# Kernel optimization log

Hardware: AMD Instinct MI355X
Metric: run time of the kernel (lower is better)

## Reference

```python
import jax, jax.numpy as jnp
import numpy as np

BASIS_PRIMES = (2, 3, 5, 7, 11, 13, 17, 19, 23, 29)


def _build_resonance(max_seq):
    # p-adic valuations v_p(n) for n = 1..max_seq, each basis prime (vectorized LUT build)
    n = np.arange(1, max_seq + 1, dtype=np.int64)
    vals = np.zeros((max_seq, len(BASIS_PRIMES)), dtype=np.float32)
    for j, p in enumerate(BASIS_PRIMES):
        m = n.copy()
        while True:
            div = (m % p) == 0
            if not div.any():
                break
            vals[div, j] += 1.0
            m = np.where(div, m // p, m)
    # resonance(a,b) = sum_i min(v_{p_i}(a), v_{p_i}(b))  -> [T, T]
    res = np.zeros((max_seq, max_seq), dtype=np.float32)
    for j in range(len(BASIS_PRIMES)):
        vj = vals[:, j]
        res += np.minimum(vj[:, None], vj[None, :])
    causal = np.tril(np.ones((max_seq, max_seq), dtype=bool))
    allowed = ((res > 0) | np.eye(max_seq, dtype=bool)) & causal
    bias = (np.log1p(res) * allowed).astype(np.float32)
    return bias, allowed


def setup_inputs() -> dict:
    B, T, d_model, head_size, max_seq = 8, 2048, 1024, 128, 2048
    key = jax.random.key(0)
    kx, kq, kk, kv = jax.random.split(key, 4)
    bound = 1.0 / np.sqrt(d_model)  # torch Linear default init range
    x = jax.random.normal(kx, (B, T, d_model), dtype=jnp.float32)
    Wq = jax.random.uniform(kq, (head_size, d_model), jnp.float32, -bound, bound)
    Wk = jax.random.uniform(kk, (head_size, d_model), jnp.float32, -bound, bound)
    Wv = jax.random.uniform(kv, (head_size, d_model), jnp.float32, -bound, bound)
    bias, allowed = _build_resonance(max_seq)
    return {
        "x": x, "Wq": Wq, "Wk": Wk, "Wv": Wv,
        "resonance_bias": jnp.asarray(bias),
        "allowed": jnp.asarray(allowed),
    }


def reference(x, Wq, Wk, Wv, resonance_bias, allowed):
    B, T, C = x.shape
    q = jnp.einsum('btc,hc->bth', x, Wq)
    k = jnp.einsum('btc,hc->bth', x, Wk)
    v = jnp.einsum('btc,hc->bth', x, Wv)
    # NOTE: original scales by C**-0.5 where C = d_model (input channels)
    wei = jnp.einsum('bth,bsh->bts', q, k) * (C ** -0.5)
    wei = wei + resonance_bias[:T, :T]
    neg = jnp.finfo(wei.dtype).min
    wei = jnp.where(allowed[:T, :T], wei, neg)
    wei = jax.nn.softmax(wei, axis=-1)  # dropout is identity in eval mode
    return jnp.einsum('bts,bsh->bth', wei, v)
```

## Files before the change

kernel.cpp:

```cpp
#include <hip/hip_runtime.h>
#include <hip/hip_bf16.h>
#include <stdint.h>

typedef float f32x4  __attribute__((ext_vector_type(4)));
typedef short s16x8  __attribute__((ext_vector_type(8)));
typedef short s16x4  __attribute__((ext_vector_type(4)));
typedef unsigned short u16x8 __attribute__((ext_vector_type(8)));

#define MFMA16(A,B,C) __builtin_amdgcn_mfma_f32_16x16x32_bf16((A),(B),(C),0,0,0)

__device__ __forceinline__ short f2bf(float f) {
    uint32_t u = __float_as_uint(f);
    u += 0x7FFFu + ((u >> 16) & 1u);
    return (short)(u >> 16);
}
__device__ __forceinline__ float bf2f(unsigned short u) {
    return __uint_as_float(((uint32_t)u) << 16);
}
__device__ __forceinline__ int cum_jobs(int qt) {
  int h = qt >> 1;
  return (qt & 1) ? (h + 1) * (h + 1) : h * (h + 1);
}

#define OFF_PB   0u
#define OFF_WPK  8388608u
#define OFF_PQ   9175040u
#define OFF_PK   13369344u
#define OFF_PV   17563648u
#define OFF_PML  21757952u
#define OFF_PO   22863872u
#define WS_SPLIT 60096512u

__global__ __launch_bounds__(256) void pack_misc_kernel(
    const float* __restrict__ wq, const float* __restrict__ wk,
    const float* __restrict__ wv, const float* __restrict__ bias,
    short* __restrict__ Wpk, short* __restrict__ pb) {
  const int tid = threadIdx.x, wid = tid >> 6, lane = tid & 63;
  const int g = lane >> 4, c4 = lane & 15;
  if (blockIdx.x < 192) {
    const int idx = blockIdx.x * 4 + wid;
    const int im = idx >> 8, rest = idx & 255;
    const int ntl = rest >> 5, k32 = rest & 31;
    const float* w = (im == 0) ? wq : (im == 1) ? wk : wv;
    const float* p = w + (size_t)(ntl * 16 + c4) * 1024 + k32 * 32 + 4 * g;
    f32x4 lo = *(const f32x4*)p;
    f32x4 hi = *(const f32x4*)(p + 16);
    s16x8 o = { f2bf(lo[0]), f2bf(lo[1]), f2bf(lo[2]), f2bf(lo[3]),
                f2bf(hi[0]), f2bf(hi[1]), f2bf(hi[2]), f2bf(hi[3]) };
    *(s16x8*)(Wpk + (size_t)idx * 512 + lane * 8) = o;
  } else {
    const int idx = (blockIdx.x - 192) * 4 + wid;
    const int t16 = idx >> 6, s32 = idx & 63;
    const int t = t16 * 16 + c4;
    const int sb = s32 * 32 + 4 * g;
    const float* p = bias + (size_t)t * 2048 + sb;
    f32x4 lo = *(const f32x4*)p;
    f32x4 hi = *(const f32x4*)(p + 16);
    s16x8 o;
    #pragma unroll
    for (int i = 0; i < 4; ++i) {
      int s0 = sb + i, s1 = sb + 16 + i;
      bool ok0 = (s0 <= t) && (s0 == t || lo[i] > 0.f);
      bool ok1 = (s1 <= t) && (s1 == t || hi[i] > 0.f);
      o[i]     = f2bf(ok0 ? lo[i] : -1e30f);
      o[4 + i] = f2bf(ok1 ? hi[i] : -1e30f);
    }
    *(s16x8*)(pb + (size_t)idx * 512 + lane * 8) = o;
  }
}

__global__ __launch_bounds__(256, 2) void qkv_gemm8_kernel(
    const float* __restrict__ x, const short* __restrict__ Wpk,
    short* __restrict__ pq, short* __restrict__ pk, short* __restrict__ pv) {
  __shared__ short lx[2][1024];
  const int tid = threadIdx.x, wid = tid >> 6, lane = tid & 63;
  const int g = lane >> 4, c4 = lane & 15;
  const int L8 = lane * 8;
  const int t2 = blockIdx.x;
  const int b = t2 >> 6;
  const int srow = tid >> 3, scg = tid & 7;
  const float* xs = x + (size_t)(t2 * 32 + srow) * 1024 + scg * 4;
  const int swoff = (srow >> 4) * 512 + (((scg & 3) * 16 + (srow & 15)) * 8)
                  + (scg >> 2) * 4;
  {
    f32x4 xv = *(const f32x4*)xs;
    s16x4 sv = { f2bf(xv[0]), f2bf(xv[1]), f2bf(xv[2]), f2bf(xv[3]) };
    *(s16x4*)&lx[0][swoff] = sv;
  }
  __syncthreads();

  if (wid < 2) {
    const short* wp = Wpk + (size_t)(wid * 256) * 512 + L8;
    f32x4 acc0[8], acc1[8];
    #pragma unroll
    for (int i = 0; i < 8; ++i) {
      acc0[i] = (f32x4){0.f, 0.f, 0.f, 0.f};
      acc1[i] = (f32x4){0.f, 0.f, 0.f, 0.f};
    }
    for (int k = 0; k < 32; ++k) {
      f32x4 xn;
      if (k < 31) xn = *(const f32x4*)(xs + (size_t)(k + 1) * 32);
      s16x8 wf[8];
      #pragma unroll
      for (int nt = 0; nt < 8; ++nt)
        wf[nt] = *(const s16x8*)(wp + (size_t)(nt * 32 + k) * 512);
      const short* lb = &lx[k & 1][0];
      s16x8 xf0 = *(const s16x8*)(lb + L8);
      s16x8 xf1 = *(const s16x8*)(lb + 512 + L8);
      #pragma unroll
      for (int nt = 0; nt < 8; ++nt) {
        acc0[nt] = MFMA16(wf[nt], xf0, acc0[nt]);
        acc1[nt] = MFMA16(wf[nt], xf1, acc1[nt]);
      }
      if (k < 31) {
        s16x4 sv = { f2bf(xn[0]), f2bf(xn[1]), f2bf(xn[2]), f2bf(xn[3]) };
        *(s16x4*)&lx[(k + 1) & 1][swoff] = sv;
      }
      __syncthreads();
    }
    short* __restrict__ o = wid ? pk : pq;
    const int loc0 = (t2 & 63) * 2;
    #pragma unroll
    for (int f = 0; f < 4; ++f) {
      s16x8 fr0 = { f2bf(acc0[2*f][0]),   f2bf(acc0[2*f][1]),
                    f2bf(acc0[2*f][2]),   f2bf(acc0[2*f][3]),
                    f2bf(acc0[2*f+1][0]), f2bf(acc0[2*f+1][1]),
                    f2bf(acc0[2*f+1][2]), f2bf(acc0[2*f+1][3]) };
      *(s16x8*)(o + (size_t)(b * 512 + loc0 * 4 + f) * 512 + L8) = fr0;
      s16x8 fr1 = { f2bf(acc1[2*f][0]),   f2bf(acc1[2*f][1]),
                    f2bf(acc1[2*f][2]),   f2bf(acc1[2*f][3]),
                    f2bf(acc1[2*f+1][0]), f2bf(acc1[2*f+1][1]),
                    f2bf(acc1[2*f+1][2]), f2bf(acc1[2*f+1][3]) };
      *(s16x8*)(o + (size_t)(b * 512 + (loc0 + 1) * 4 + f) * 512 + L8) = fr1;
    }
  } else {
    const int ntoff = (wid - 2) * 4;
    const short* wp = Wpk + (size_t)(512 + ntoff * 32) * 512 + L8;
    f32x4 acc0[4], acc1[4];
    #pragma unroll
    for (int i = 0; i < 4; ++i) {
      acc0[i] = (f32x4){0.f, 0.f, 0.f, 0.f};
      acc1[i] = (f32x4){0.f, 0.f, 0.f, 0.f};
    }
    for (int k = 0; k < 32; ++k) {
      f32x4 xn;
      if (k < 31) xn = *(const f32x4*)(xs + (size_t)(k + 1) * 32);
      s16x8 wf[4];
      #pragma unroll
      for (int j = 0; j < 4; ++j)
        wf[j] = *(const s16x8*)(wp + (size_t)(j * 32 + k) * 512);
      const short* lb = &lx[k & 1][0];
      s16x8 xf0 = *(const s16x8*)(lb + L8);
      s16x8 xf1 = *(const s16x8*)(lb + 512 + L8);
      #pragma unroll
      for (int j = 0; j < 4; ++j) {
        acc0[j] = MFMA16(xf0, wf[j], acc0[j]);
        acc1[j] = MFMA16(xf1, wf[j], acc1[j]);
      }
      if (k < 31) {
        s16x4 sv = { f2bf(xn[0]), f2bf(xn[1]), f2bf(xn[2]), f2bf(xn[3]) };
        *(s16x4*)&lx[(k + 1) & 1][swoff] = sv;
      }
      __syncthreads();
    }
    const int s32l = t2 & 63;
    #pragma unroll
    for (int j = 0; j < 4; ++j) {
      s16x8 fr = { f2bf(acc0[j][0]), f2bf(acc0[j][1]),
                   f2bf(acc0[j][2]), f2bf(acc0[j][3]),
                   f2bf(acc1[j][0]), f2bf(acc1[j][1]),
                   f2bf(acc1[j][2]), f2bf(acc1[j][3]) };
      *(s16x8*)(pv + (size_t)(b * 512 + s32l * 8 + ntoff + j) * 512 + L8) = fr;
    }
  }
}

template<bool SPLIT>
__global__ __launch_bounds__(128) void attn_kernel(
    const short* __restrict__ pq, const short* __restrict__ pk,
    const short* __restrict__ pv, const short* __restrict__ pb,
    float* __restrict__ out, float* __restrict__ part_ml,
    short* __restrict__ part_o) {
  int qt, c;
  if (SPLIT) {
    const int i = blockIdx.x;
    int h = (int)sqrtf((float)i);
    while (h * h > i) --h;
    while ((h + 1) * (h + 1) <= i) ++h;
    if (i < h * (h + 1)) { qt = 2 * h - 1; c = i - h * h; }
    else                 { qt = 2 * h;     c = i - h * (h + 1); }
  } else {
    qt = blockIdx.x; c = 0;
  }
  const int n = (qt >> 1) + 1;
  const int tid = threadIdx.x;
  const int wid = tid >> 6, lane = tid & 63;
  const int g = lane >> 4, c4 = lane & 15;
  const int b = blockIdx.y;
  const int q16a = qt * 4 + wid * 2;
  const int L8 = lane * 8;

  s16x8 qfa[4], qfb[4];
  #pragma unroll
  for (int f = 0; f < 4; ++f) {
    qfa[f] = *(const s16x8*)(pq + (size_t)(b * 512 + q16a * 4 + f) * 512 + L8);
    qfb[f] = *(const s16x8*)(pq + (size_t)(b * 512 + (q16a + 1) * 4 + f) * 512 + L8);
  }

  float m0 = -1e30f, l0 = 0.f, m1 = -1e30f, l1 = 0.f;
  f32x4 acc0[8], acc1[8];
  #pragma unroll
  for (int i = 0; i < 8; ++i) {
    acc0[i] = (f32x4){0.f, 0.f, 0.f, 0.f};
    acc1[i] = (f32x4){0.f, 0.f, 0.f, 0.f};
  }

  const int q_hi_w = qt * 64 + wid * 32 + 32;
  const int s_begin = SPLIT ? c * 128 : 0;
  const int s_stop  = min(SPLIT ? s_begin + 128 : (1 << 30), q_hi_w);

  for (int s0 = s_begin; s0 < s_stop; s0 += 32) {
    const int s16i = s0 >> 4, s32 = s0 >> 5;
    const short* kbase = pk + (size_t)(b * 512 + s16i * 4) * 512 + L8;
    const short* vbase = pv + (size_t)(b * 512 + s32 * 8) * 512 + L8;
    s16x8 kf0[4], kf1[4];
    #pragma unroll
    for (int f = 0; f < 4; ++f) {
      kf0[f] = *(const s16x8*)(kbase + (size_t)f * 512);
      kf1[f] = *(const s16x8*)(kbase + (size_t)(4 + f) * 512);
    }
    u16x8 bva = *(const u16x8*)(pb + (size_t)(q16a * 64 + s32) * 512 + L8);
    u16x8 bvb = *(const u16x8*)(pb + (size_t)((q16a + 1) * 64 + s32) * 512 + L8);
    f32x4 s0a = (f32x4){0.f,0.f,0.f,0.f}, s1a = (f32x4){0.f,0.f,0.f,0.f};
    f32x4 s0b = (f32x4){0.f,0.f,0.f,0.f}, s1b = (f32x4){0.f,0.f,0.f,0.f};
    __builtin_amdgcn_s_setprio(1);
    #pragma unroll
    for (int f = 0; f < 4; ++f) {
      s0a = MFMA16(kf0[f], qfa[f], s0a);
      s1a = MFMA16(kf1[f], qfa[f], s1a);
      s0b = MFMA16(kf0[f], qfb[f], s0b);
      s1b = MFMA16(kf1[f], qfb[f], s1b);
    }
    __builtin_amdgcn_s_setprio(0);
    float va[8], vb[8];
    #pragma unroll
    for (int st = 0; st < 2; ++st)
      #pragma unroll
      for (int r = 0; r < 4; ++r) {
        va[st * 4 + r] = (st ? s1a[r] : s0a[r]) * 0.03125f + bf2f(bva[st * 4 + r]);
        vb[st * 4 + r] = (st ? s1b[r] : s0b[r]) * 0.03125f + bf2f(bvb[st * 4 + r]);
      }
    float mva = va[0], mvb = vb[0];
    #pragma unroll
    for (int i = 1; i < 8; ++i) { mva = fmaxf(mva, va[i]); mvb = fmaxf(mvb, vb[i]); }
    mva = fmaxf(mva, __shfl_xor(mva, 16)); mva = fmaxf(mva, __shfl_xor(mva, 32));
    mvb = fmaxf(mvb, __shfl_xor(mvb, 16)); mvb = fmaxf(mvb, __shfl_xor(mvb, 32));
    if (!__all((mva <= m0 + 8.f) && (mvb <= m1 + 8.f))) {
      float mn0 = fmaxf(m0, mva), mn1 = fmaxf(m1, mvb);
      float a0 = __expf(m0 - mn0), a1 = __expf(m1 - mn1);
      l0 *= a0; l1 *= a1; m0 = mn0; m1 = mn1;
      float ar0[4], ar1[4];
      #pragma unroll
      for (int r = 0; r < 4; ++r) {
        ar0[r] = __shfl(a0, (lane & 48) | (4 * g + r));
        ar1[r] = __shfl(a1, (lane & 48) | (4 * g + r));
      }
      #pragma unroll
      for (int nt = 0; nt < 8; ++nt)
        #pragma unroll
        for (int r = 0; r < 4; ++r) {
          acc0[nt][r] *= ar0[r];
          acc1[nt][r] *= ar1[r];
        }
    }
    float pa8[8], pb8[8], psa = 0.f, psb = 0.f;
    #pragma unroll
    for (int i = 0; i < 8; ++i) {
      pa8[i] = (va[i] > -1e29f) ? __expf(va[i] - m0) : 0.f;  psa += pa8[i];
      pb8[i] = (vb[i] > -1e29f) ? __expf(vb[i] - m1) : 0.f;  psb += pb8[i];
    }
    psa += __shfl_xor(psa, 16); psa += __shfl_xor(psa, 32); l0 += psa;
    psb += __shfl_xor(psb, 16); psb += __shfl_xor(psb, 32); l1 += psb;
    s16x8 paf = { f2bf(pa8[0]), f2bf(pa8[1]), f2bf(pa8[2]), f2bf(pa8[3]),
                  f2bf(pa8[4]), f2bf(pa8[5]), f2bf(pa8[6]), f2bf(pa8[7]) };
    s16x8 pbf = { f2bf(pb8[0]), f2bf(pb8[1]), f2bf(pb8[2]), f2bf(pb8[3]),
                  f2bf(pb8[4]), f2bf(pb8[5]), f2bf(pb8[6]), f2bf(pb8[7]) };
    __builtin_amdgcn_s_setprio(1);
    #pragma unroll
    for (int nt = 0; nt < 8; ++nt) {
      s16x8 vf = *(const s16x8*)(vbase + (size_t)nt * 512);
      acc0[nt] = MFMA16(paf, vf, acc0[nt]);
      acc1[nt] = MFMA16(pbf, vf, acc1[nt]);
    }
    __builtin_amdgcn_s_setprio(0);
  }

  if (!SPLIT || n == 1) {
    float li0 = 1.f / l0, li1 = 1.f / l1;
    float lr0[4], lr1[4];
    #pragma unroll
    for (int r = 0; r < 4; ++r) {
      lr0[r] = __shfl(li0, (lane & 48) | (4 * g + r));
      lr1[r] = __shfl(li1, (lane & 48) | (4 * g + r));
    }
    const int row0 = qt * 64 + wid * 32;
    #pragma unroll
    for (int nt = 0; nt < 8; ++nt)
      #pragma unroll
      for (int r = 0; r < 4; ++r) {
        out[(size_t)(b * 2048 + row0 + 4 * g + r) * 128 + 16 * nt + c4] =
            acc0[nt][r] * lr0[r];
        out[(size_t)(b * 2048 + row0 + 16 + 4 * g + r) * 128 + 16 * nt + c4] =
            acc1[nt][r] * lr1[r];
      }
  } else {
    const int slot = b * 270 + cum_jobs(qt) - 2 + c;
    short* po = part_o + (size_t)slot * 8192 + (size_t)(wid * 8) * 512 + L8;
    #pragma unroll
    for (int nt = 0; nt < 8; ++nt) {
      s16x8 fr = { f2bf(acc0[nt][0]), f2bf(acc0[nt][1]),
                   f2bf(acc0[nt][2]), f2bf(acc0[nt][3]),
                   f2bf(acc1[nt][0]), f2bf(acc1[nt][1]),
                   f2bf(acc1[nt][2]), f2bf(acc1[nt][3]) };
      *(s16x8*)(po + (size_t)nt * 512) = fr;
    }
    if (lane < 16) {
      part_ml[slot * 128 + wid * 32 + c4]           = m0;
      part_ml[slot * 128 + wid * 32 + 16 + c4]      = m1;
      part_ml[slot * 128 + 64 + wid * 32 + c4]      = l0;
      part_ml[slot * 128 + 64 + wid * 32 + 16 + c4] = l1;
    }
  }
}

__global__ __launch_bounds__(256) void combine_kernel(
    const float* __restrict__ part_ml, const unsigned short* __restrict__ part_o,
    float* __restrict__ out) {
  const int qt = 2 + blockIdx.x;
  const int b = blockIdx.y;
  const int n = (qt >> 1) + 1;
  const int slot0 = b * 270 + cum_jobs(qt) - 2;
  const int tid = threadIdx.x;

  __shared__ float scl[16][64];
  if (tid < 64) {
    const int r = tid;
    float M = -1e30f;
    for (int cc = 0; cc < n; ++cc)
      M = fmaxf(M, part_ml[(size_t)(slot0 + cc) * 128 + r]);
    float L = 0.f;
    for (int cc = 0; cc < n; ++cc)
      L += part_ml[(size_t)(slot0 + cc) * 128 + 64 + r] *
           __expf(part_ml[(size_t)(slot0 + cc) * 128 + r] - M);
    float inv = 1.f / L;
    for (int cc = 0; cc < n; ++cc)
      scl[cc][r] = __expf(part_ml[(size_t)(slot0 + cc) * 128 + r] - M) * inv;
  }
  __syncthreads();
  const int fgr = tid >> 6, lane = tid & 63;
  const int g = lane >> 4, c4 = lane & 15;
  for (int ff = fgr; ff < 16; ff += 4) {
    const int rbase = (ff >> 3) * 32 + 4 * g;
    const int col = (ff & 7) * 16 + c4;
    float o[8] = {0.f,0.f,0.f,0.f,0.f,0.f,0.f,0.f};
    for (int cc = 0; cc < n; ++cc) {
      u16x8 v = *(const u16x8*)(part_o +
          (size_t)(slot0 + cc) * 8192 + (size_t)ff * 512 + lane * 8);
      #pragma unroll
      for (int j = 0; j < 8; ++j)
        o[j] += bf2f(v[j]) * scl[cc][rbase + (j >> 2) * 16 + (j & 3)];
    }
    #pragma unroll
    for (int j = 0; j < 8; ++j) {
      const int row = rbase + (j >> 2) * 16 + (j & 3);
      out[(size_t)(b * 2048 + qt * 64 + row) * 128 + col] = o[j];
    }
  }
}

extern "C" void kernel_launch(void* const* d_in, const int* in_sizes, int n_in,
                              void* d_out, int out_size, void* d_ws, size_t ws_size,
                              hipStream_t stream) {
  const float* x    = (const float*)d_in[0];
  const float* wq   = (const float*)d_in[1];
  const float* wk   = (const float*)d_in[2];
  const float* wv   = (const float*)d_in[3];
  const float* bias = (const float*)d_in[4];

  char* ws = (char*)d_ws;
  short* pb      = (short*)(ws + OFF_PB);
  short* Wpk     = (short*)(ws + OFF_WPK);
  short* pq      = (short*)(ws + OFF_PQ);
  short* pk      = (short*)(ws + OFF_PK);
  short* pv      = (short*)(ws + OFF_PV);
  float* part_ml = (float*)(ws + OFF_PML);
  short* part_o  = (short*)(ws + OFF_PO);
  float* outp    = (float*)d_out;

  pack_misc_kernel<<<2240, 256, 0, stream>>>(wq, wk, wv, bias, Wpk, pb);
  qkv_gemm8_kernel<<<512, 256, 0, stream>>>(x, Wpk, pq, pk, pv);

  if (ws_size >= WS_SPLIT) {
    attn_kernel<true><<<dim3(272, 8), 128, 0, stream>>>(
        pq, pk, pv, pb, outp, part_ml, part_o);
    combine_kernel<<<dim3(30, 8), 256, 0, stream>>>(
        part_ml, (const unsigned short*)part_o, outp);
  } else {
    attn_kernel<false><<<dim3(32, 8), 128, 0, stream>>>(
        pq, pk, pv, pb, outp, part_ml, part_o);
  }
}
```

Before: 104.1 us.

## Restructure QKV GEMM to 8 waves with larger K-chunks and swizzled LDS

Rewrites the QKV projection kernel so each block runs 8 waves instead of 4. Each wave now handles one 16-row group instead of two, which halves per-wave accumulator state and raises the number of waves available to hide latency. The x tile is staged in LDS in 256-wide K chunks, double-buffered, with an XOR swizzle to avoid bank conflicts. This cuts the number of __syncthreads from 32 to 4. The cost is that each wave reloads the weight fragments from global memory per row group, which doubles weight traffic relative to reusing them across two row groups.

Result: slower. 116.6 us (+12.1%).

```diff
diff --git a/kernel.cpp b/kernel.cpp
--- a/kernel.cpp
+++ b/kernel.cpp
@@ -69,108 +69,115 @@
   }
 }
 
-__global__ __launch_bounds__(256, 2) void qkv_gemm8_kernel(
+__global__ __launch_bounds__(512, 4) void qkv_gemm9_kernel(
     const float* __restrict__ x, const short* __restrict__ Wpk,
     short* __restrict__ pq, short* __restrict__ pk, short* __restrict__ pv) {
-  __shared__ short lx[2][1024];
+  __shared__ short lx[16384];
   const int tid = threadIdx.x, wid = tid >> 6, lane = tid & 63;
-  const int g = lane >> 4, c4 = lane & 15;
+  const int g = lane >> 4;
   const int L8 = lane * 8;
   const int t2 = blockIdx.x;
   const int b = t2 >> 6;
-  const int srow = tid >> 3, scg = tid & 7;
-  const float* xs = x + (size_t)(t2 * 32 + srow) * 1024 + scg * 4;
-  const int swoff = (srow >> 4) * 512 + (((scg & 3) * 16 + (srow & 15)) * 8)
-                  + (scg >> 2) * 4;
+
+  const int sk32 = lane >> 3, sg = lane & 3, shi = (lane >> 2) & 1;
+  int lidx[4]; const float* gp[4];
+  #pragma unroll
+  for (int i = 0; i < 4; ++i) {
+    int s = sg * 16 + wid + 8 * (i & 1);
+    int p = s ^ sk32 ^ (sg << 1);
+    lidx[i] = sk32 * 1024 + (i >> 1) * 512 + p * 8 + shi * 4;
+    gp[i] = x + (size_t)(t2 * 32 + wid + 8 * i) * 1024 + lane * 4;
+  }
+
+  f32x4 acc[8];
+  #pragma unroll
+  for (int i = 0; i < 8; ++i) acc[i] = (f32x4){0.f, 0.f, 0.f, 0.f};
+
   {
-    f32x4 xv = *(const f32x4*)xs;
-    s16x4 sv = { f2bf(xv[0]), f2bf(xv[1]), f2bf(xv[2]), f2bf(xv[3]) };
-    *(s16x4*)&lx[0][swoff] = sv;
+    f32x4 y0 = *(const f32x4*)gp[0];
+    f32x4 y1 = *(const f32x4*)gp[1];
+    f32x4 y2 = *(const f32x4*)gp[2];
+    f32x4 y3 = *(const f32x4*)gp[3];
+    s16x4 v0 = { f2bf(y0[0]), f2bf(y0[1]), f2bf(y0[2]), f2bf(y0[3]) };
+    s16x4 v1 = { f2bf(y1[0]), f2bf(y1[1]), f2bf(y1[2]), f2bf(y1[3]) };
+    s16x4 v2 = { f2bf(y2[0]), f2bf(y2[1]), f2bf(y2[2]), f2bf(y2[3]) };
+    s16x4 v3 = { f2bf(y3[0]), f2bf(y3[1]), f2bf(y3[2]), f2bf(y3[3]) };
+    *(s16x4*)&lx[lidx[0]] = v0;
+    *(s16x4*)&lx[lidx[1]] = v1;
+    *(s16x4*)&lx[lidx[2]] = v2;
+    *(s16x4*)&lx[lidx[3]] = v3;
   }
   __syncthreads();
 
-  if (wid < 2) {
-    const short* wp = Wpk + (size_t)(wid * 256) * 512 + L8;
-    f32x4 acc0[8], acc1[8];
-    #pragma unroll
-    for (int i = 0; i < 8; ++i) {
-      acc0[i] = (f32x4){0.f, 0.f, 0.f, 0.f};
-      acc1[i] = (f32x4){0.f, 0.f, 0.f, 0.f};
-    }
-    for (int k = 0; k < 32; ++k) {
-      f32x4 xn;
-      if (k < 31) xn = *(const f32x4*)(xs + (size_t)(k + 1) * 32);
-      s16x8 wf[8];
-      #pragma unroll
-      for (int nt = 0; nt < 8; ++nt)
-        wf[nt] = *(const s16x8*)(wp + (size_t)(nt * 32 + k) * 512);
-      const short* lb = &lx[k & 1][0];
-      s16x8 xf0 = *(const s16x8*)(lb + L8);
-      s16x8 xf1 = *(const s16x8*)(lb + 512 + L8);
-      #pragma unroll
-      for (int nt = 0; nt < 8; ++nt) {
-        acc0[nt] = MFMA16(wf[nt], xf0, acc0[nt]);
-        acc1[nt] = MFMA16(wf[nt], xf1, acc1[nt]);
+  #pragma unroll
+  for (int kbi = 0; kbi < 4; ++kbi) {
+    const int cur = (kbi & 1) * 8192, nxt = ((kbi + 1) & 1) * 8192;
+    f32x4 y0, y1, y2, y3;
+    if (kbi < 3) {
+      y0 = *(const f32x4*)(gp[0] + (kbi + 1) * 256);
+      y1 = *(const f32x4*)(gp[1] + (kbi + 1) * 256);
+      y2 = *(const f32x4*)(gp[2] + (kbi + 1) * 256);
+      y3 = *(const f32x4*)(gp[3] + (kbi + 1) * 256);
+    }
+    if (wid < 4) {
+      const int im = wid >> 1, rg = wid & 1;
+      const short* wp = Wpk + (size_t)(im * 256) * 512 + L8;
+      #pragma unroll
+      for (int kk = 0; kk < 8; ++kk) {
+        s16x8 xf = *(const s16x8*)&lx[cur + kk * 1024 + rg * 512 +
+                                      (lane ^ kk ^ (g << 1)) * 8];
+        #pragma unroll
+        for (int nt = 0; nt < 8; ++nt) {
+          s16x8 wf = *(const s16x8*)(wp + (size_t)(nt * 32 + kbi * 8 + kk) * 512);
+          acc[nt] = MFMA16(wf, xf, acc[nt]);
+        }
       }
-      if (k < 31) {
-        s16x4 sv = { f2bf(xn[0]), f2bf(xn[1]), f2bf(xn[2]), f2bf(xn[3]) };
-        *(s16x4*)&lx[(k + 1) & 1][swoff] = sv;
+    } else {
+      const int rg = (wid >> 1) & 1, ntb = (wid & 1) * 4;
+      const short* wp = Wpk + (size_t)(512 + ntb * 32) * 512 + L8;
+      #pragma unroll
+      for (int kk = 0; kk < 8; ++kk) {
+        s16x8 xf = *(const s16x8*)&lx[cur + kk * 1024 + rg * 512 +
+                                      (lane ^ kk ^ (g << 1)) * 8];
+        #pragma unroll
+        for (int j = 0; j < 4; ++j) {
+          s16x8 wf = *(const s16x8*)(wp + (size_t)(j * 32 + kbi * 8 + kk) * 512);
+          acc[j] = MFMA16(xf, wf, acc[j]);
+        }
       }
-      __syncthreads();
-    }
-    short* __restrict__ o = wid ? pk : pq;
-    const int loc0 = (t2 & 63) * 2;
+    }
+    if (kbi < 3) {
+      s16x4 v0 = { f2bf(y0[0]), f2bf(y0[1]), f2bf(y0[2]), f2bf(y0[3]) };
+      s16x4 v1 = { f2bf(y1[0]), f2bf(y1[1]), f2bf(y1[2]), f2bf(y1[3]) };
+      s16x4 v2 = { f2bf(y2[0]), f2bf(y2[1]), f2bf(y2[2]), f2bf(y2[3]) };
+      s16x4 v3 = { f2bf(y3[0]), f2bf(y3[1]), f2bf(y3[2]), f2bf(y3[3]) };
+      *(s16x4*)&lx[nxt + lidx[0]] = v0;
+      *(s16x4*)&lx[nxt + lidx[1]] = v1;
+      *(s16x4*)&lx[nxt + lidx[2]] = v2;
+      *(s16x4*)&lx[nxt + lidx[3]] = v3;
+    }
+    __syncthreads();
+  }
+
+  if (wid < 4) {
+    short* __restrict__ o = (wid >> 1) ? pk : pq;
+    const int q16l = (t2 & 63) * 2 + (wid & 1);
     #pragma unroll
     for (int f = 0; f < 4; ++f) {
-      s16x8 fr0 = { f2bf(acc0[2*f][0]),   f2bf(acc0[2*f][1]),
-                    f2bf(acc0[2*f][2]),   f2bf(acc0[2*f][3]),
-                    f2bf(acc0[2*f+1][0]), f2bf(acc0[2*f+1][1]),
-                    f2bf(acc0[2*f+1][2]), f2bf(acc0[2*f+1][3]) };
-      *(s16x8*)(o + (size_t)(b * 512 + loc0 * 4 + f) * 512 + L8) = fr0;
-      s16x8 fr1 = { f2bf(acc1[2*f][0]),   f2bf(acc1[2*f][1]),
-                    f2bf(acc1[2*f][2]),   f2bf(acc1[2*f][3]),
-                    f2bf(acc1[2*f+1][0]), f2bf(acc1[2*f+1][1]),
-                    f2bf(acc1[2*f+1][2]), f2bf(acc1[2*f+1][3]) };
-      *(s16x8*)(o + (size_t)(b * 512 + (loc0 + 1) * 4 + f) * 512 + L8) = fr1;
+      s16x8 fr = { f2bf(acc[2*f][0]),   f2bf(acc[2*f][1]),
+                   f2bf(acc[2*f][2]),   f2bf(acc[2*f][3]),
+                   f2bf(acc[2*f+1][0]), f2bf(acc[2*f+1][1]),
+                   f2bf(acc[2*f+1][2]), f2bf(acc[2*f+1][3]) };
+      *(s16x8*)(o + (size_t)(b * 512 + q16l * 4 + f) * 512 + L8) = fr;
     }
   } else {
-    const int ntoff = (wid - 2) * 4;
-    const short* wp = Wpk + (size_t)(512 + ntoff * 32) * 512 + L8;
-    f32x4 acc0[4], acc1[4];
-    #pragma unroll
-    for (int i = 0; i < 4; ++i) {
-      acc0[i] = (f32x4){0.f, 0.f, 0.f, 0.f};
-      acc1[i] = (f32x4){0.f, 0.f, 0.f, 0.f};
-    }
-    for (int k = 0; k < 32; ++k) {
-      f32x4 xn;
-      if (k < 31) xn = *(const f32x4*)(xs + (size_t)(k + 1) * 32);
-      s16x8 wf[4];
-      #pragma unroll
-      for (int j = 0; j < 4; ++j)
-        wf[j] = *(const s16x8*)(wp + (size_t)(j * 32 + k) * 512);
-      const short* lb = &lx[k & 1][0];
-      s16x8 xf0 = *(const s16x8*)(lb + L8);
-      s16x8 xf1 = *(const s16x8*)(lb + 512 + L8);
-      #pragma unroll
-      for (int j = 0; j < 4; ++j) {
-        acc0[j] = MFMA16(xf0, wf[j], acc0[j]);
-        acc1[j] = MFMA16(xf1, wf[j], acc1[j]);
-      }
-      if (k < 31) {
-        s16x4 sv = { f2bf(xn[0]), f2bf(xn[1]), f2bf(xn[2]), f2bf(xn[3]) };
-        *(s16x4*)&lx[(k + 1) & 1][swoff] = sv;
-      }
-      __syncthreads();
-    }
+    const int rg = (wid >> 1) & 1, ntb = (wid & 1) * 4;
     const int s32l = t2 & 63;
     #pragma unroll
     for (int j = 0; j < 4; ++j) {
-      s16x8 fr = { f2bf(acc0[j][0]), f2bf(acc0[j][1]),
-                   f2bf(acc0[j][2]), f2bf(acc0[j][3]),
-                   f2bf(acc1[j][0]), f2bf(acc1[j][1]),
-                   f2bf(acc1[j][2]), f2bf(acc1[j][3]) };
-      *(s16x8*)(pv + (size_t)(b * 512 + s32l * 8 + ntoff + j) * 512 + L8) = fr;
+      s16x4 fr = { f2bf(acc[j][0]), f2bf(acc[j][1]),
+                   f2bf(acc[j][2]), f2bf(acc[j][3]) };
+      *(s16x4*)(pv + (size_t)(b * 512 + s32l * 8 + ntb + j) * 512 + L8 + rg * 4) = fr;
     }
   }
 }
@@ -398,7 +405,7 @@
   float* outp    = (float*)d_out;
 
   pack_misc_kernel<<<2240, 256, 0, stream>>>(wq, wk, wv, bias, Wpk, pb);
-  qkv_gemm8_kernel<<<512, 256, 0, stream>>>(x, Wpk, pq, pk, pv);
+  qkv_gemm9_kernel<<<512, 512, 0, stream>>>(x, Wpk, pq, pk, pv);
 
   if (ws_size >= WS_SPLIT) {
     attn_kernel<true><<<dim3(272, 8), 128, 0, stream>>>(
```
